# Optimization experiments

Measured on AMD Instinct MI355X. Metric: run time of the kernel, lower is better.

The kernel has to match this reference:

```python
import jax, jax.numpy as jnp
import numpy as np

NUM_HEADS = 8
CHUNK = 64
TOP_K = 5


def setup_inputs() -> dict:
    key = jax.random.key(0)
    ks = jax.random.split(key, 5)
    D = 512
    x = jax.random.normal(ks[0], (1, 2048, D), dtype=jnp.float32)
    s = 0.02
    Wq = jax.random.normal(ks[1], (D, D), dtype=jnp.float32) * s
    Wk = jax.random.normal(ks[2], (D, D), dtype=jnp.float32) * s
    Wv = jax.random.normal(ks[3], (D, D), dtype=jnp.float32) * s
    Wo = jax.random.normal(ks[4], (D, D), dtype=jnp.float32) * s
    return {"x": x, "Wq": Wq, "Wk": Wk, "Wv": Wv, "Wo": Wo}


def reference(x, Wq, Wk, Wv, Wo):
    B, S, D = x.shape
    H = NUM_HEADS
    hd = D // H
    scale = hd ** -0.5
    C = S // CHUNK  # number of chunks

    def split_heads(t):
        return t.reshape(B, S, H, hd).transpose(0, 2, 1, 3)  # [B,H,S,hd]

    Q = split_heads(x @ Wq)
    K = split_heads(x @ Wk)
    V = split_heads(x @ Wv)

    # chunked K/V: [B,H,C,chunk,hd]
    Kc = K.reshape(B, H, C, CHUNK, hd)
    Vc = V.reshape(B, H, C, CHUNK, hd)

    # chunk descriptors: mean-pooled keys per chunk -> [B,H,C,hd]
    chunk_keys = Kc.mean(axis=3)

    # route each query to top-k chunks by scaled similarity
    sims = jnp.einsum('bhsd,bhcd->bhsc', Q, chunk_keys) * scale  # [B,H,S,C]
    _, idx = jax.lax.top_k(sims, TOP_K)  # [B,H,S,K]

    # gather selected K/V chunk blocks: [B,H,S,K,chunk,hd]
    idx_flat = idx.reshape(B, H, S * TOP_K)[:, :, :, None, None]
    Kg = jnp.take_along_axis(Kc, idx_flat, axis=2).reshape(B, H, S, TOP_K, CHUNK, hd)
    Vg = jnp.take_along_axis(Vc, idx_flat, axis=2).reshape(B, H, S, TOP_K, CHUNK, hd)

    # sparse block attention over the K*chunk gathered keys per query
    scores = jnp.einsum('bhsd,bhskcd->bhskc', Q, Kg) * scale
    attn = jax.nn.softmax(scores.reshape(B, H, S, TOP_K * CHUNK), axis=-1)
    attn = attn.reshape(B, H, S, TOP_K, CHUNK)
    out = jnp.einsum('bhskc,bhskcd->bhsd', attn, Vg)  # [B,H,S,hd]

    out = out.transpose(0, 2, 1, 3).reshape(B, S, D)
    return out @ Wo
```

## Files before the change

### kernel.cpp

```cpp
#include <hip/hip_runtime.h>
#include <hip/hip_bf16.h>
#include <math.h>

#define S_LEN 2048
#define D_DIM 512
#define H_NUM 8
#define HD    64
#define C_NUM 32
#define TOPK  5
#define SCALE 0.125f
#define QCAP  1024
#define ATILES 16

typedef __attribute__((ext_vector_type(8))) short bf16x8;
typedef __attribute__((ext_vector_type(4))) float f32x4;
typedef __attribute__((ext_vector_type(4))) unsigned short us4;

__device__ __forceinline__ unsigned short f2b(float f) {
    __hip_bfloat16 h = __float2bfloat16(f);
    unsigned short u;
    __builtin_memcpy(&u, &h, 2);
    return u;
}
__device__ __forceinline__ bf16x8 pack8(float4 a, float4 b) {
    bf16x8 r;
    r[0] = (short)f2b(a.x); r[1] = (short)f2b(a.y);
    r[2] = (short)f2b(a.z); r[3] = (short)f2b(a.w);
    r[4] = (short)f2b(b.x); r[5] = (short)f2b(b.y);
    r[6] = (short)f2b(b.z); r[7] = (short)f2b(b.w);
    return r;
}
__device__ __forceinline__ float b2f(unsigned short u) {
    __hip_bfloat16 h;
    __builtin_memcpy(&h, &u, 2);
    return __bfloat162float(h);
}

#define BM 64
#define BN 64
#define BK 32

__device__ __forceinline__ void gemm_body(const float* __restrict__ A,
                                          const float* __restrict__ B,
                                          float* __restrict__ C,
                                          int M, int N, int K,
                                          int bx, int by) {
    __shared__ float As[BK][BM + 4];
    __shared__ float Bs[BK][BN];

    const int t  = threadIdx.x;
    const int tx = t & 15;
    const int ty = t >> 4;
    const int m0 = by * BM;
    const int n0 = bx * BN;

    float4 acc0 = make_float4(0.f,0.f,0.f,0.f);
    float4 acc1 = make_float4(0.f,0.f,0.f,0.f);
    float4 acc2 = make_float4(0.f,0.f,0.f,0.f);
    float4 acc3 = make_float4(0.f,0.f,0.f,0.f);

    const int ar = t >> 3;
    const int ac = (t & 7) * 4;
    const int br = t >> 4;
    const int bc = (t & 15) * 4;

    float4 a0, a1, b0, b1;
    auto LD = [&](int k0) {
        a0 = *(const float4*)&A[(size_t)(m0 + ar)      * K + k0 + ac];
        a1 = *(const float4*)&A[(size_t)(m0 + ar + 32) * K + k0 + ac];
        b0 = *(const float4*)&B[(size_t)(k0 + br)      * N + n0 + bc];
        b1 = *(const float4*)&B[(size_t)(k0 + br + 16) * N + n0 + bc];
    };

    LD(0);
    for (int k0 = 0; k0 < K; k0 += BK) {
        __syncthreads();
        As[ac+0][ar]    = a0.x; As[ac+1][ar]    = a0.y; As[ac+2][ar]    = a0.z; As[ac+3][ar]    = a0.w;
        As[ac+0][ar+32] = a1.x; As[ac+1][ar+32] = a1.y; As[ac+2][ar+32] = a1.z; As[ac+3][ar+32] = a1.w;
        *(float4*)&Bs[br][bc]      = b0;
        *(float4*)&Bs[br + 16][bc] = b1;
        __syncthreads();

        if (k0 + BK < K) LD(k0 + BK);

        #pragma unroll
        for (int kk = 0; kk < BK; ++kk) {
            float4 a = *(const float4*)&As[kk][ty * 4];
            float4 b = *(const float4*)&Bs[kk][tx * 4];
            acc0.x += a.x*b.x; acc0.y += a.x*b.y; acc0.z += a.x*b.z; acc0.w += a.x*b.w;
            acc1.x += a.y*b.x; acc1.y += a.y*b.y; acc1.z += a.y*b.z; acc1.w += a.y*b.w;
            acc2.x += a.z*b.x; acc2.y += a.z*b.y; acc2.z += a.z*b.z; acc2.w += a.z*b.w;
            acc3.x += a.w*b.x; acc3.y += a.w*b.y; acc3.z += a.w*b.z; acc3.w += a.w*b.w;
        }
    }

    *(float4*)&C[(size_t)(m0 + ty*4 + 0) * N + n0 + tx*4] = acc0;
    *(float4*)&C[(size_t)(m0 + ty*4 + 1) * N + n0 + tx*4] = acc1;
    *(float4*)&C[(size_t)(m0 + ty*4 + 2) * N + n0 + tx*4] = acc2;
    *(float4*)&C[(size_t)(m0 + ty*4 + 3) * N + n0 + tx*4] = acc3;
}

__device__ __forceinline__ void gemm_v_body(const float* __restrict__ A,
                                            const float* __restrict__ B,
                                            unsigned short* __restrict__ C,
                                            int M, int N, int K,
                                            int bx, int by) {
    __shared__ unsigned short Asv[64][72];
    __shared__ unsigned short Bsv[64][72];

    const int t  = threadIdx.x;
    const int m0 = by * 64;
    const int n0 = bx * 64;
    const int rl = t >> 2;
    const int c4 = (t & 3) * 16;

    const int lane = t & 63, w = t >> 6, lr = lane & 15, quad = lane >> 4;

    f32x4 acc[4] = {{0.f,0.f,0.f,0.f},{0.f,0.f,0.f,0.f},
                    {0.f,0.f,0.f,0.f},{0.f,0.f,0.f,0.f}};

    float4 fa[4], fb[4];
    auto LDA = [&](int k0) {
        const float* p = &A[(size_t)(m0 + rl) * K + k0 + c4];
        fa[0] = *(const float4*)&p[0];  fa[1] = *(const float4*)&p[4];
        fa[2] = *(const float4*)&p[8];  fa[3] = *(const float4*)&p[12];
    };
    auto LDB = [&](int k0) {
        const float* p = &B[(size_t)(k0 + rl) * N + n0 + c4];
        fb[0] = *(const float4*)&p[0];  fb[1] = *(const float4*)&p[4];
        fb[2] = *(const float4*)&p[8];  fb[3] = *(const float4*)&p[12];
    };

    LDA(0); LDB(0);
    for (int k0 = 0; k0 < K; k0 += 64) {
        __syncthreads();
        *(bf16x8*)&Asv[rl][c4]     = pack8(fa[0], fa[1]);
        *(bf16x8*)&Asv[rl][c4 + 8] = pack8(fa[2], fa[3]);
        #pragma unroll
        for (int f = 0; f < 4; ++f) {
            float4 v = fb[f];
            Bsv[c4 + f*4 + 0][rl] = f2b(v.x);
            Bsv[c4 + f*4 + 1][rl] = f2b(v.y);
            Bsv[c4 + f*4 + 2][rl] = f2b(v.z);
            Bsv[c4 + f*4 + 3][rl] = f2b(v.w);
        }
        __syncthreads();

        if (k0 + 64 < K) { LDA(k0 + 64); LDB(k0 + 64); }

        bf16x8 a0 = *(const bf16x8*)&Asv[w * 16 + lr][quad * 8];
        bf16x8 a1 = *(const bf16x8*)&Asv[w * 16 + lr][32 + quad * 8];
        #pragma unroll
        for (int nt = 0; nt < 4; ++nt) {
            bf16x8 b0 = *(const bf16x8*)&Bsv[nt * 16 + lr][quad * 8];
            bf16x8 b1 = *(const bf16x8*)&Bsv[nt * 16 + lr][32 + quad * 8];
            acc[nt] = __builtin_amdgcn_mfma_f32_16x16x32_bf16(a0, b0, acc[nt], 0, 0, 0);
            acc[nt] = __builtin_amdgcn_mfma_f32_16x16x32_bf16(a1, b1, acc[nt], 0, 0, 0);
        }
    }

    #pragma unroll
    for (int nt = 0; nt < 4; ++nt)
        #pragma unroll
        for (int r = 0; r < 4; ++r) {
            int m = m0 + w * 16 + quad * 4 + r;
            int n = n0 + nt * 16 + lr;
            C[(size_t)m * N + n] = f2b(acc[nt][r]);
        }
}

__global__ __launch_bounds__(256) void proj4(const float* __restrict__ x,
                                             const float* __restrict__ Wq,
                                             const float* __restrict__ Wk,
                                             const float* __restrict__ Wv,
                                             float* __restrict__ Qf,
                                             unsigned short* __restrict__ Kbf,
                                             unsigned short* __restrict__ Vbf,
                                             float* __restrict__ xbar,
                                             int* __restrict__ cur) {
    if (blockIdx.z == 0) {
        gemm_body(x, Wq, Qf, S_LEN, D_DIM, D_DIM, blockIdx.x, blockIdx.y);
    } else if (blockIdx.z == 1) {
        gemm_v_body(x, Wk, Kbf, S_LEN, D_DIM, D_DIM, blockIdx.x, blockIdx.y);
    } else if (blockIdx.z == 2) {
        gemm_v_body(x, Wv, Vbf, S_LEN, D_DIM, D_DIM, blockIdx.x, blockIdx.y);
    } else {
        int t = threadIdx.x;
        if (blockIdx.x == 0 && blockIdx.y == 0) cur[t] = 0;
        int flat = (blockIdx.y * 8 + blockIdx.x) * 256 + t;
        if (flat < C_NUM * D_DIM) {
            int c = flat >> 9, d = flat & 511;
            const float* p = x + (size_t)c * 64 * D_DIM + d;
            float s = 0.f;
            #pragma unroll
            for (int r = 0; r < 64; ++r) s += p[(size_t)r * D_DIM];
            xbar[flat] = s * (1.0f / 64.0f);
        }
    }
}

__global__ __launch_bounds__(256) void ck_kernel(const float* __restrict__ xbar,
                                                 const float* __restrict__ Wk,
                                                 float* __restrict__ ck) {
    __shared__ float xl[512];
    const int c = blockIdx.x, t = threadIdx.x;
    xl[t]       = xbar[c * 512 + t];
    xl[t + 256] = xbar[c * 512 + t + 256];
    __syncthreads();
    float s0 = 0.f, s1 = 0.f;
    #pragma unroll 8
    for (int j = 0; j < 512; ++j) {
        float xv = xl[j];
        s0 += xv * Wk[(size_t)j * 512 + t];
        s1 += xv * Wk[(size_t)j * 512 + t + 256];
    }
    ck[c * 512 + t]       = s0;
    ck[c * 512 + t + 256] = s1;
}

__global__ __launch_bounds__(256) void sims_topk(const float* __restrict__ Q,
                                                 const float* __restrict__ ck,
                                                 int* __restrict__ cur,
                                                 unsigned short* __restrict__ qlist) {
    __shared__ float qtile[64][68];
    __shared__ float cks[32][68];
    __shared__ float simsb[64][36];
    __shared__ int   lds_cnt[32];
    __shared__ int   lds_base[32];

    const int t  = threadIdx.x;
    const int s0 = blockIdx.x * 64;
    const int h  = blockIdx.y;

    if (t < 32) lds_cnt[t] = 0;

    {
        int r = t >> 2;
        #pragma unroll
        for (int i = 0; i < 4; ++i) {
            int cf4 = (t & 3) * 4 + i;
            *(float4*)&qtile[r][cf4 * 4] =
                *(const float4*)&Q[(size_t)(s0 + r) * D_DIM + h * HD + cf4 * 4];
        }
    }
    for (int i = t; i < C_NUM * 16; i += 256) {
        int c = i >> 4, df4 = i & 15;
        *(float4*)&cks[c][df4 * 4] =
            *(const float4*)&ck[(size_t)c * D_DIM + h * HD + df4 * 4];
    }
    __syncthreads();

    {
        const int sl = t >> 2, g = t & 3;
        float sa[8] = {0.f,0.f,0.f,0.f,0.f,0.f,0.f,0.f};
        #pragma unroll
        for (int d4 = 0; d4 < 16; ++d4) {
            float4 q4 = *(const float4*)&qtile[sl][d4 * 4];
            #pragma unroll
            for (int j = 0; j < 8; ++j) {
                float4 c4 = *(const float4*)&cks[g * 8 + j][d4 * 4];
                sa[j] += q4.x*c4.x + q4.y*c4.y + q4.z*c4.z + q4.w*c4.w;
            }
        }
        *(float4*)&simsb[sl][g*8 + 0] = make_float4(sa[0], sa[1], sa[2], sa[3]);
        *(float4*)&simsb[sl][g*8 + 4] = make_float4(sa[4], sa[5], sa[6], sa[7]);
    }
    __syncthreads();

    int csel[TOPK], lpos[TOPK];
    if (t < 64) {
        float sv[32];
        #pragma unroll
        for (int cq = 0; cq < 8; ++cq) {
            float4 v = *(const float4*)&simsb[t][cq * 4];
            sv[cq*4+0] = v.x; sv[cq*4+1] = v.y; sv[cq*4+2] = v.z; sv[cq*4+3] = v.w;
        }
        #pragma unroll
        for (int k = 0; k < TOPK; ++k) {
            float best = -INFINITY; int bi = 0;
            #pragma unroll
            for (int cc = 0; cc < 32; ++cc) {
                bool gt = sv[cc] > best;
                best = gt ? sv[cc] : best;
                bi   = gt ? cc : bi;
            }
            #pragma unroll
            for (int cc = 0; cc < 32; ++cc)
                if (cc == bi) sv[cc] = -INFINITY;
            csel[k] = bi;
            lpos[k] = atomicAdd(&lds_cnt[bi], 1);
        }
    }
    __syncthreads();

    if (t < 32) lds_base[t] = atomicAdd(&cur[h * 32 + t], lds_cnt[t]);
    __syncthreads();

    if (t < 64) {
        #pragma unroll
        for (int k = 0; k < TOPK; ++k) {
            int c = csel[k];
            int pos = lds_base[c] + lpos[k];
            if (pos < QCAP)
                qlist[(size_t)(h * 32 + c) * QCAP + pos] =
                    (unsigned short)((s0 + t) | (k << 11));
        }
    }
}

__global__ __launch_bounds__(256) void moc_attn6c(const float* __restrict__ Qf,
                                                  const unsigned short* __restrict__ Kbf,
                                                  const unsigned short* __restrict__ Vbf,
                                                  const int* __restrict__ cnt,
                                                  const unsigned short* __restrict__ qlist,
                                                  float* __restrict__ lpart,
                                                  float* __restrict__ Opart) {
    __shared__ unsigned short Qs[64][72];
    __shared__ unsigned short Ks[64][72];
    __shared__ unsigned short VT[64][72];
    __shared__ unsigned short Ps[64][72];
    __shared__ unsigned short slist[64];

    const int hc = blockIdx.y;
    const int h  = hc >> 5;
    const int c  = hc & 31;
    const int g  = blockIdx.x;
    const int t  = threadIdx.x;

    const int count = min(cnt[hc], QCAP);
    const int base  = g * 64;
    if (base >= count) return;
    const int lim = min(count - base, 64);

    const unsigned short* Kb = Kbf + ((size_t)c * 64) * D_DIM + h * HD;
    const unsigned short* Vb = Vbf + ((size_t)c * 64) * D_DIM + h * HD;
    const unsigned short* list = qlist + (size_t)hc * QCAP + base;

    {
        const int j  = t >> 2;
        const int d0 = (t & 3) * 16;

        const unsigned short* kr = Kb + (size_t)j * D_DIM + d0;
        *(bf16x8*)&Ks[j][d0]     = *(const bf16x8*)&kr[0];
        *(bf16x8*)&Ks[j][d0 + 8] = *(const bf16x8*)&kr[8];

        const unsigned short* vr = Vb + (size_t)j * D_DIM + d0;
        bf16x8 v0 = *(const bf16x8*)&vr[0];
        bf16x8 v1 = *(const bf16x8*)&vr[8];
        #pragma unroll
        for (int i = 0; i < 8; ++i) {
            VT[d0 + i][j]     = (unsigned short)v0[i];
            VT[d0 + 8 + i][j] = (unsigned short)v1[i];
        }

        unsigned short pv = (j < lim) ? list[j] : (unsigned short)0xFFFF;
        if ((t & 3) == 0) slist[j] = pv;
        int s = (pv == 0xFFFF) ? 0 : (int)(pv & 2047);
        const float* qr = Qf + (size_t)s * D_DIM + h * HD + d0;
        float4 q0 = *(const float4*)&qr[0],  q1 = *(const float4*)&qr[4];
        float4 q2 = *(const float4*)&qr[8],  q3 = *(const float4*)&qr[12];
        *(bf16x8*)&Qs[j][d0]     = pack8(q0, q1);
        *(bf16x8*)&Qs[j][d0 + 8] = pack8(q2, q3);
    }
    __syncthreads();

    const int lane = t & 63;
    const int w    = t >> 6;
    const int lr   = lane & 15;
    const int quad = lane >> 4;

    bf16x8 aq0 = *(const bf16x8*)&Qs[w * 16 + lr][quad * 8];
    bf16x8 aq1 = *(const bf16x8*)&Qs[w * 16 + lr][32 + quad * 8];

    f32x4 acc[4];
    #pragma unroll
    for (int kt = 0; kt < 4; ++kt) {
        bf16x8 b0 = *(const bf16x8*)&Ks[kt * 16 + lr][quad * 8];
        bf16x8 b1 = *(const bf16x8*)&Ks[kt * 16 + lr][32 + quad * 8];
        f32x4 z = {0.f, 0.f, 0.f, 0.f};
        z = __builtin_amdgcn_mfma_f32_16x16x32_bf16(aq0, b0, z, 0, 0, 0);
        z = __builtin_amdgcn_mfma_f32_16x16x32_bf16(aq1, b1, z, 0, 0, 0);
        acc[kt] = z;
    }

    unsigned short pb[4][4];
    float dsum[4] = {0.f, 0.f, 0.f, 0.f};
    #pragma unroll
    for (int kt = 0; kt < 4; ++kt) {
        #pragma unroll
        for (int r = 0; r < 4; ++r) {
            unsigned short u = f2b(__expf(acc[kt][r] * SCALE));
            pb[kt][r] = u;
            dsum[r] += b2f(u);
        }
    }
    #pragma unroll
    for (int r = 0; r < 4; ++r) {
        float v = dsum[r];
        v += __shfl_xor(v, 1, 64);
        v += __shfl_xor(v, 2, 64);
        v += __shfl_xor(v, 4, 64);
        v += __shfl_xor(v, 8, 64);
        dsum[r] = v;
    }
    if (lr == 0) {
        #pragma unroll
        for (int r = 0; r < 4; ++r) {
            unsigned short sv = slist[w * 16 + quad * 4 + r];
            if (sv != 0xFFFF) {
                int kk = sv >> 11, s = sv & 2047;
                lpart[((size_t)kk * H_NUM + h) * S_LEN + s] = dsum[r];
            }
        }
    }

    #pragma unroll
    for (int kt = 0; kt < 4; ++kt)
        #pragma unroll
        for (int r = 0; r < 4; ++r)
            Ps[w * 16 + quad * 4 + r][kt * 16 + lr] = pb[kt][r];

    bf16x8 ap0 = *(const bf16x8*)&Ps[w * 16 + lr][quad * 8];
    bf16x8 ap1 = *(const bf16x8*)&Ps[w * 16 + lr][32 + quad * 8];

    #pragma unroll
    for (int dt = 0; dt < 4; ++dt) {
        bf16x8 b0 = *(const bf16x8*)&VT[dt * 16 + lr][quad * 8];
        bf16x8 b1 = *(const bf16x8*)&VT[dt * 16 + lr][32 + quad * 8];
        f32x4 z = {0.f, 0.f, 0.f, 0.f};
        z = __builtin_amdgcn_mfma_f32_16x16x32_bf16(ap0, b0, z, 0, 0, 0);
        z = __builtin_amdgcn_mfma_f32_16x16x32_bf16(ap1, b1, z, 0, 0, 0);
        #pragma unroll
        for (int r = 0; r < 4; ++r) {
            unsigned short sv = slist[w * 16 + quad * 4 + r];
            if (sv != 0xFFFF) {
                int kk = sv >> 11, s = sv & 2047;
                Opart[((((size_t)kk * H_NUM + h) * S_LEN + s) * HD) + dt * 16 + lr] = z[r];
            }
        }
    }
}

__global__ __launch_bounds__(256) void reduce_norm(const float4* __restrict__ Opart4,
                                                   const float* __restrict__ lpart,
                                                   unsigned short* __restrict__ Obn) {
    int i = blockIdx.x * 256 + threadIdx.x;
    int s    = i >> 7;
    int col4 = i & 127;
    int h    = col4 >> 4;
    int f4   = col4 & 15;
    float4 acc = make_float4(0.f,0.f,0.f,0.f);
    float  den = 0.f;
    #pragma unroll
    for (int k = 0; k < TOPK; ++k) {
        size_t slot = ((size_t)k * H_NUM + h) * S_LEN + s;
        float4 v = Opart4[slot * 16 + f4];
        acc.x += v.x; acc.y += v.y; acc.z += v.z; acc.w += v.w;
        den += lpart[slot];
    }
    float inv = 1.0f / den;
    us4 o;
    o[0] = f2b(acc.x * inv); o[1] = f2b(acc.y * inv);
    o[2] = f2b(acc.z * inv); o[3] = f2b(acc.w * inv);
    *(us4*)&Obn[(size_t)i * 4] = o;
}

__global__ __launch_bounds__(256) void gemm_out(const unsigned short* __restrict__ Obn,
                                                const float* __restrict__ Wo,
                                                float* __restrict__ out) {
    __shared__ unsigned short As[64][72];
    __shared__ unsigned short Bs[64][72];

    const int t  = threadIdx.x;
    const int m0 = blockIdx.y * 64;
    const int n0 = blockIdx.x * 64;
    const int rl = t >> 2;
    const int c4 = (t & 3) * 16;
    const int N = D_DIM, K = D_DIM;

    const int lane = t & 63, w = t >> 6, lr = lane & 15, quad = lane >> 4;

    f32x4 acc[4] = {{0.f,0.f,0.f,0.f},{0.f,0.f,0.f,0.f},
                    {0.f,0.f,0.f,0.f},{0.f,0.f,0.f,0.f}};

    bf16x8 ba[2]; float4 fb[4];
    auto LDA = [&](int k0) {
        const unsigned short* p = &Obn[(size_t)(m0 + rl) * K + k0 + c4];
        ba[0] = *(const bf16x8*)&p[0];
        ba[1] = *(const bf16x8*)&p[8];
    };
    auto LDB = [&](int k0) {
        const float* p = &Wo[(size_t)(k0 + rl) * N + n0 + c4];
        fb[0] = *(const float4*)&p[0];  fb[1] = *(const float4*)&p[4];
        fb[2] = *(const float4*)&p[8];  fb[3] = *(const float4*)&p[12];
    };

    LDA(0); LDB(0);
    for (int k0 = 0; k0 < K; k0 += 64) {
        __syncthreads();
        *(bf16x8*)&As[rl][c4]     = ba[0];
        *(bf16x8*)&As[rl][c4 + 8] = ba[1];
        #pragma unroll
        for (int f = 0; f < 4; ++f) {
            float4 v = fb[f];
            Bs[c4 + f*4 + 0][rl] = f2b(v.x);
            Bs[c4 + f*4 + 1][rl] = f2b(v.y);
            Bs[c4 + f*4 + 2][rl] = f2b(v.z);
            Bs[c4 + f*4 + 3][rl] = f2b(v.w);
        }
        __syncthreads();

        if (k0 + 64 < K) { LDA(k0 + 64); LDB(k0 + 64); }

        bf16x8 a0 = *(const bf16x8*)&As[w * 16 + lr][quad * 8];
        bf16x8 a1 = *(const bf16x8*)&As[w * 16 + lr][32 + quad * 8];
        #pragma unroll
        for (int nt = 0; nt < 4; ++nt) {
            bf16x8 b0 = *(const bf16x8*)&Bs[nt * 16 + lr][quad * 8];
            bf16x8 b1 = *(const bf16x8*)&Bs[nt * 16 + lr][32 + quad * 8];
            acc[nt] = __builtin_amdgcn_mfma_f32_16x16x32_bf16(a0, b0, acc[nt], 0, 0, 0);
            acc[nt] = __builtin_amdgcn_mfma_f32_16x16x32_bf16(a1, b1, acc[nt], 0, 0, 0);
        }
    }

    #pragma unroll
    for (int nt = 0; nt < 4; ++nt)
        #pragma unroll
        for (int r = 0; r < 4; ++r) {
            int m = m0 + w * 16 + quad * 4 + r;
            int n = n0 + nt * 16 + lr;
            out[(size_t)m * N + n] = acc[nt][r];
        }
}

extern "C" void kernel_launch(void* const* d_in, const int* in_sizes, int n_in,
                              void* d_out, int out_size, void* d_ws, size_t ws_size,
                              hipStream_t stream) {
    const float* x  = (const float*)d_in[0];
    const float* Wq = (const float*)d_in[1];
    const float* Wk = (const float*)d_in[2];
    const float* Wv = (const float*)d_in[3];
    const float* Wo = (const float*)d_in[4];
    float* out = (float*)d_out;

    const size_t SD = (size_t)S_LEN * D_DIM;
    float* Qf = (float*)d_ws;
    unsigned short* Kbf = (unsigned short*)(Qf + SD);
    unsigned short* Vbf = Kbf + SD;
    float* xbar = (float*)(Vbf + SD);
    float* ck   = xbar + (size_t)C_NUM * D_DIM;
    float* lpart = ck + (size_t)C_NUM * D_DIM;
    int*   curb  = (int*)(lpart + (size_t)TOPK * H_NUM * S_LEN);
    unsigned short* qlst = (unsigned short*)(curb + 256);
    float* Opart = (float*)(qlst + (size_t)256 * QCAP);
    unsigned short* Obn = (unsigned short*)Qf;

    dim3 pgrid(D_DIM / 64, S_LEN / 64, 4);
    proj4<<<pgrid, 256, 0, stream>>>(x, Wq, Wk, Wv, Qf, Kbf, Vbf, xbar, curb);

    ck_kernel<<<C_NUM, 256, 0, stream>>>(xbar, Wk, ck);

    dim3 rgrid(S_LEN / 64, H_NUM);
    sims_topk<<<rgrid, 256, 0, stream>>>(Qf, ck, curb, qlst);

    dim3 agrid(ATILES, H_NUM * C_NUM);
    moc_attn6c<<<agrid, 256, 0, stream>>>(Qf, Kbf, Vbf, curb, qlst, lpart, Opart);

    reduce_norm<<<(int)(SD / 4 / 256), 256, 0, stream>>>((const float4*)Opart, lpart, Obn);

    dim3 ogrid(D_DIM / 64, S_LEN / 64);
    gemm_out<<<ogrid, 256, 0, stream>>>(Obn, Wo, out);
}
```

Baseline: 168.3 us.

## Split Q projection into its own kernel and fuse chunk-key computation into K/V GEMM

The combined projection kernel is split so the fp32 Q GEMM runs as a standalone kernel. The K/V bf16 GEMMs now share a launch with the blocks that mean-pool x per chunk and compute the chunk keys, which removes the separate ck_kernel launch and the xbar round trip through global memory. The launch count stays the same, but the chunk-key work now overlaps the K/V GEMM instead of running serially after it. The catch is that the Q GEMM no longer overlaps K/V, and most z=2 blocks exit immediately.

```diff
diff --git a/kernel.cpp b/kernel.cpp
--- a/kernel.cpp
+++ b/kernel.cpp
@@ -40,19 +40,18 @@
 #define BN 64
 #define BK 32
 
-__device__ __forceinline__ void gemm_body(const float* __restrict__ A,
-                                          const float* __restrict__ B,
-                                          float* __restrict__ C,
-                                          int M, int N, int K,
-                                          int bx, int by) {
+__global__ __launch_bounds__(256) void gemm_q(const float* __restrict__ A,
+                                              const float* __restrict__ B,
+                                              float* __restrict__ C) {
     __shared__ float As[BK][BM + 4];
     __shared__ float Bs[BK][BN];
 
     const int t  = threadIdx.x;
     const int tx = t & 15;
     const int ty = t >> 4;
-    const int m0 = by * BM;
-    const int n0 = bx * BN;
+    const int m0 = blockIdx.y * BM;
+    const int n0 = blockIdx.x * BN;
+    const int N = D_DIM, K = D_DIM;
 
     float4 acc0 = make_float4(0.f,0.f,0.f,0.f);
     float4 acc1 = make_float4(0.f,0.f,0.f,0.f);
@@ -169,53 +168,45 @@
         }
 }
 
-__global__ __launch_bounds__(256) void proj4(const float* __restrict__ x,
-                                             const float* __restrict__ Wq,
-                                             const float* __restrict__ Wk,
-                                             const float* __restrict__ Wv,
-                                             float* __restrict__ Qf,
-                                             unsigned short* __restrict__ Kbf,
-                                             unsigned short* __restrict__ Vbf,
-                                             float* __restrict__ xbar,
-                                             int* __restrict__ cur) {
-    if (blockIdx.z == 0) {
-        gemm_body(x, Wq, Qf, S_LEN, D_DIM, D_DIM, blockIdx.x, blockIdx.y);
-    } else if (blockIdx.z == 1) {
-        gemm_v_body(x, Wk, Kbf, S_LEN, D_DIM, D_DIM, blockIdx.x, blockIdx.y);
-    } else if (blockIdx.z == 2) {
-        gemm_v_body(x, Wv, Vbf, S_LEN, D_DIM, D_DIM, blockIdx.x, blockIdx.y);
-    } else {
-        int t = threadIdx.x;
-        if (blockIdx.x == 0 && blockIdx.y == 0) cur[t] = 0;
-        int flat = (blockIdx.y * 8 + blockIdx.x) * 256 + t;
-        if (flat < C_NUM * D_DIM) {
-            int c = flat >> 9, d = flat & 511;
-            const float* p = x + (size_t)c * 64 * D_DIM + d;
-            float s = 0.f;
-            #pragma unroll
-            for (int r = 0; r < 64; ++r) s += p[(size_t)r * D_DIM];
-            xbar[flat] = s * (1.0f / 64.0f);
-        }
-    }
-}
-
-__global__ __launch_bounds__(256) void ck_kernel(const float* __restrict__ xbar,
-                                                 const float* __restrict__ Wk,
-                                                 float* __restrict__ ck) {
-    __shared__ float xl[512];
-    const int c = blockIdx.x, t = threadIdx.x;
-    xl[t]       = xbar[c * 512 + t];
-    xl[t + 256] = xbar[c * 512 + t + 256];
-    __syncthreads();
-    float s0 = 0.f, s1 = 0.f;
-    #pragma unroll 8
-    for (int j = 0; j < 512; ++j) {
-        float xv = xl[j];
-        s0 += xv * Wk[(size_t)j * 512 + t];
-        s1 += xv * Wk[(size_t)j * 512 + t + 256];
-    }
-    ck[c * 512 + t]       = s0;
-    ck[c * 512 + t + 256] = s1;
+__global__ __launch_bounds__(256) void gemm_kv_ck(const float* __restrict__ x,
+                                                  const float* __restrict__ Wk,
+                                                  const float* __restrict__ Wv,
+                                                  unsigned short* __restrict__ Kbf,
+                                                  unsigned short* __restrict__ Vbf,
+                                                  float* __restrict__ ck,
+                                                  int* __restrict__ cur) {
+    if (blockIdx.z == 2) {
+        if (blockIdx.x != 0) return;
+        __shared__ float xl[512];
+        const int c = blockIdx.y;
+        const int t = threadIdx.x;
+        if (c == 0) cur[t] = 0;
+
+        const float* xp = x + (size_t)c * 64 * D_DIM;
+        float s0 = 0.f, s1 = 0.f;
+        #pragma unroll
+        for (int r = 0; r < 64; ++r) {
+            s0 += xp[(size_t)r * D_DIM + t];
+            s1 += xp[(size_t)r * D_DIM + t + 256];
+        }
+        xl[t]       = s0 * (1.0f / 64.0f);
+        xl[t + 256] = s1 * (1.0f / 64.0f);
+        __syncthreads();
+
+        float a0 = 0.f, a1 = 0.f;
+        #pragma unroll 8
+        for (int j = 0; j < 512; ++j) {
+            float xv = xl[j];
+            a0 += xv * Wk[(size_t)j * 512 + t];
+            a1 += xv * Wk[(size_t)j * 512 + t + 256];
+        }
+        ck[c * 512 + t]       = a0;
+        ck[c * 512 + t + 256] = a1;
+        return;
+    }
+    const float* W = (blockIdx.z == 0) ? Wk : Wv;
+    unsigned short* C = (blockIdx.z == 0) ? Kbf : Vbf;
+    gemm_v_body(x, W, C, S_LEN, D_DIM, D_DIM, blockIdx.x, blockIdx.y);
 }
 
 __global__ __launch_bounds__(256) void sims_topk(const float* __restrict__ Q,
@@ -547,18 +538,18 @@
     float* Qf = (float*)d_ws;
     unsigned short* Kbf = (unsigned short*)(Qf + SD);
     unsigned short* Vbf = Kbf + SD;
-    float* xbar = (float*)(Vbf + SD);
-    float* ck   = xbar + (size_t)C_NUM * D_DIM;
+    float* ck   = (float*)(Vbf + SD);
     float* lpart = ck + (size_t)C_NUM * D_DIM;
     int*   curb  = (int*)(lpart + (size_t)TOPK * H_NUM * S_LEN);
     unsigned short* qlst = (unsigned short*)(curb + 256);
     float* Opart = (float*)(qlst + (size_t)256 * QCAP);
     unsigned short* Obn = (unsigned short*)Qf;
 
-    dim3 pgrid(D_DIM / 64, S_LEN / 64, 4);
-    proj4<<<pgrid, 256, 0, stream>>>(x, Wq, Wk, Wv, Qf, Kbf, Vbf, xbar, curb);
-
-    ck_kernel<<<C_NUM, 256, 0, stream>>>(xbar, Wk, ck);
+    dim3 qgrid(D_DIM / BN, S_LEN / BM);
+    gemm_q<<<qgrid, 256, 0, stream>>>(x, Wq, Qf);
+
+    dim3 kvgrid(D_DIM / 64, S_LEN / 64, 3);
+    gemm_kv_ck<<<kvgrid, 256, 0, stream>>>(x, Wk, Wv, Kbf, Vbf, ck, curb);
 
     dim3 rgrid(S_LEN / 64, H_NUM);
     sims_topk<<<rgrid, 256, 0, stream>>>(Qf, ck, curb, qlst);
```

Result: no change. 167.1 us (-0.7%).
